# Kernel tuning notes

Hardware: AMD Instinct MI355X
Metric: run time of the kernel (lower is better)

## Reference

```python
import jax, jax.numpy as jnp
import numpy as np

B, C, H, W = 32, 48, 64, 128
K = 5  # conv kernel size (1x5 / 5x1)


def _conv1d(x, w, b):
    # x: [B, C, L]; w: [O, I, K]; b: [O]. 'same' conv (pad 2) along L.
    y = jax.lax.conv_general_dilated(x, w, window_strides=(1,), padding=[(2, 2)],
                                     dimension_numbers=("NCH", "OIH", "NCH"))
    return y + b[None, :, None]


def setup_inputs() -> dict:
    key = jax.random.key(0)
    ks = jax.random.split(key, 7)
    s = 0.02  # small init so the 64/128-step linear recurrences stay bounded
    return {
        "x": jax.random.normal(ks[0], (B, C, H, W), dtype=jnp.float32),
        "down_w": jax.random.normal(ks[1], (C, C, K), dtype=jnp.float32) * s,
        "down_b": jax.random.normal(ks[2], (C,), dtype=jnp.float32) * s,
        "right_w": jax.random.normal(ks[3], (C, C, K), dtype=jnp.float32) * s,
        "right_b": jax.random.normal(ks[4], (C,), dtype=jnp.float32) * s,
        "left_w": jax.random.normal(ks[5], (C, C, K), dtype=jnp.float32) * s,
        "left_b": jax.random.normal(ks[6], (C,), dtype=jnp.float32) * s,
    }


def reference(x, down_w, down_b, right_w, right_b, left_w, left_b):
    Bb, Cc, Hh, Ww = x.shape

    def step(w, b):
        def f(carry, inp):
            nxt = inp + _conv1d(carry, w, b)
            return nxt, nxt
        return f

    # --- down pass: d[0]=x[0]; d[t]=x[t]+down_conv(d[t-1]) ---
    xs = jnp.moveaxis(x, 2, 0)                       # [H, B, C, W]
    d0 = xs[0]
    _, d_rest = jax.lax.scan(step(down_w, down_b), d0, xs[1:])
    D = jnp.concatenate([d0[None], d_rest], 0)       # [H, B, C, W]

    # --- up pass: faithfully uses down_conv (source quirk) with index H-3-t
    # u[0]=D[H-1]; u[k]=D[H-2-k]+down_conv(u[k-1]), k=1..H-1 (H-2-k=-1 -> D[H-1])
    seq = jnp.concatenate([D[Hh - 3::-1], D[Hh - 1:Hh]], 0)  # [H-1, B, C, W]
    u0 = D[Hh - 1]
    _, u_rest = jax.lax.scan(step(down_w, down_b), u0, seq)
    U = jnp.concatenate([u0[None], u_rest], 0)[::-1]  # U[i] = u[H-1-i]

    # --- right pass over width: r[0]=U[...,0]; r[t]=U[...,t]+right_conv(r[t-1]) ---
    ws = jnp.moveaxis(jnp.moveaxis(U, 0, 2), 3, 0)   # [W, B, C, H]
    r0 = ws[0]
    _, r_rest = jax.lax.scan(step(right_w, right_b), r0, ws[1:])
    R = jnp.concatenate([r0[None], r_rest], 0)       # [W, B, C, H]

    # --- left pass (reverse): l[0]=R[W-1]; l[k]=R[W-1-k]+left_conv(l[k-1]) ---
    l0 = R[Ww - 1]
    _, l_rest = jax.lax.scan(step(left_w, left_b), l0, R[Ww - 2::-1])
    L = jnp.concatenate([l0[None], l_rest], 0)[::-1]  # [W, B, C, H]

    return jnp.moveaxis(L, 0, 3)                     # [B, C, H, W]
```

## Files before the change

kernel.cpp:

```cpp
#include <hip/hip_runtime.h>
#include <hip/hip_bf16.h>

#define B_ 32
#define C_ 48
#define H_ 64
#define W_ 128
#define K_ 5
#define SLAB (C_*H_*W_)
#define RS 56
#define ROWS 136
#define CBUF (ROWS*RS)
#define WC (W_*C_)
#define HC (H_*C_)
#define KBN 16
#define C1ROW 135

typedef __attribute__((ext_vector_type(8))) short short8;
typedef __attribute__((ext_vector_type(16))) float f32x16;
typedef unsigned short ushort;

__device__ __forceinline__ void lbar() {
  asm volatile("s_waitcnt lgkmcnt(0)\n\ts_barrier" ::: "memory");
}

__device__ __forceinline__ unsigned short f2bf(float f) {
  union { float f; unsigned u; } v; v.f = f;
  unsigned r = v.u + 0x7fffu + ((v.u >> 16) & 1u);
  return (unsigned short)(r >> 16);
}

__device__ __forceinline__ unsigned pk2(float a, float b) {
  union { __hip_bfloat162 h; unsigned u; } z;
  z.h = __float22bfloat162_rn(float2{a, b});
  return z.u;
}

template<int NMT>
__device__ __forceinline__ void load_wA32(const float* __restrict__ wgt,
                                          const float* __restrict__ bias,
                                          short8 Aw[NMT][KBN], int mt0,
                                          int l31, int h) {
#pragma unroll
  for (int mti = 0; mti < NMT; ++mti) {
    const int m = (mt0 + mti) * 32 + l31;
#pragma unroll
    for (int kbn = 0; kbn < KBN; ++kbn) {
      short8 f;
#pragma unroll
      for (int j = 0; j < 8; ++j) {
        int kp = kbn * 16 + h * 8 + j;
        float val = 0.f;
        if (m < C_) {
          if (kp < 240) {
            int k = kp / 48, i = kp - 48 * k;
            val = wgt[m * (C_ * K_) + i * K_ + k];
          } else if (kp == 240) {
            val = bias[m];
          }
        }
        f[j] = (short)f2bf(val);
      }
      Aw[mti][kbn] = f;
    }
  }
}

__device__ __forceinline__ void loadx6(float4 xv[6], const float* __restrict__ inp,
                                       size_t inRS, int n0, int l31, int h4) {
  const float* ip = inp + (size_t)(n0 + l31) * inRS + h4;
  xv[0] = *(const float4*)(ip + 0);
  xv[1] = *(const float4*)(ip + 8);
  xv[2] = *(const float4*)(ip + 16);
  xv[3] = *(const float4*)(ip + 24);
  xv[4] = *(const float4*)(ip + 32);
  xv[5] = *(const float4*)(ip + 40);
}

__device__ __forceinline__ void stepW32(const ushort* __restrict__ scr,
                                        ushort* __restrict__ scw,
                                        const short8 Aw[2][KBN],
                                        const float4 xvc[6], float4 xvn[6],
                                        const float* __restrict__ inpn, size_t inRS,
                                        float* __restrict__ outp,
                                        int n0, int l31, int h4,
                                        const int off_r[KBN], int c1off) {
  f32x16 a00 = (f32x16)(0.0f), a01 = (f32x16)(0.0f);
  f32x16 a10 = (f32x16)(0.0f), a11 = (f32x16)(0.0f);
  const ushort* bp = scr + (size_t)n0 * RS;
#pragma unroll
  for (int kbn = 0; kbn < KBN; ++kbn) {
    int off = (kbn == 15) ? c1off : off_r[kbn];
    short8 pf = *(const short8*)(bp + off);
    if (kbn & 1) {
      a01 = __builtin_amdgcn_mfma_f32_32x32x16_bf16(Aw[0][kbn], pf, a01, 0, 0, 0);
      a11 = __builtin_amdgcn_mfma_f32_32x32x16_bf16(Aw[1][kbn], pf, a11, 0, 0, 0);
    } else {
      a00 = __builtin_amdgcn_mfma_f32_32x32x16_bf16(Aw[0][kbn], pf, a00, 0, 0, 0);
      a10 = __builtin_amdgcn_mfma_f32_32x32x16_bf16(Aw[1][kbn], pf, a10, 0, 0, 0);
    }
  }
  loadx6(xvn, inpn, inRS, n0, l31, h4);
  __builtin_amdgcn_sched_barrier(0);

  const int row = n0 + l31;
  float* op = outp + (size_t)row * C_ + h4;
  ushort* wp = scw + (size_t)(row + 2) * RS + h4;
#pragma unroll
  for (int grp = 0; grp < 6; ++grp) {
    const int g = (grp < 4) ? grp : (grp - 4);
    const int ch = ((grp < 4) ? 0 : 32) + 8 * g;
    float4 v;
    if (grp < 4) {
      v.x = a00[4*g+0] + a01[4*g+0] + xvc[grp].x;
      v.y = a00[4*g+1] + a01[4*g+1] + xvc[grp].y;
      v.z = a00[4*g+2] + a01[4*g+2] + xvc[grp].z;
      v.w = a00[4*g+3] + a01[4*g+3] + xvc[grp].w;
    } else {
      v.x = a10[4*g+0] + a11[4*g+0] + xvc[grp].x;
      v.y = a10[4*g+1] + a11[4*g+1] + xvc[grp].y;
      v.z = a10[4*g+2] + a11[4*g+2] + xvc[grp].z;
      v.w = a10[4*g+3] + a11[4*g+3] + xvc[grp].w;
    }
    *(float4*)(op + ch) = v;
    uint2 pk; pk.x = pk2(v.x, v.y); pk.y = pk2(v.z, v.w);
    *(uint2*)(wp + ch) = pk;
  }
  lbar();
}

template<int MT>
__device__ __forceinline__ void stepH32(const ushort* __restrict__ scr,
                                        ushort* __restrict__ scw,
                                        const short8 Aw[KBN],
                                        const float4 xvc[4], float4 xvn[4],
                                        const float* __restrict__ inpn, size_t inRS,
                                        float* __restrict__ outp,
                                        int n0, int l31, int h4,
                                        const int off_r[KBN], int c1off) {
  constexpr int NG = MT ? 2 : 4;
  f32x16 a0 = (f32x16)(0.0f), a1 = (f32x16)(0.0f);
  f32x16 a2 = (f32x16)(0.0f), a3 = (f32x16)(0.0f);
  const ushort* bp = scr + (size_t)n0 * RS;
#pragma unroll
  for (int kbn = 0; kbn < KBN; ++kbn) {
    int off = (kbn == 15) ? c1off : off_r[kbn];
    short8 pf = *(const short8*)(bp + off);
    switch (kbn & 3) {
      case 0: a0 = __builtin_amdgcn_mfma_f32_32x32x16_bf16(Aw[kbn], pf, a0, 0, 0, 0); break;
      case 1: a1 = __builtin_amdgcn_mfma_f32_32x32x16_bf16(Aw[kbn], pf, a1, 0, 0, 0); break;
      case 2: a2 = __builtin_amdgcn_mfma_f32_32x32x16_bf16(Aw[kbn], pf, a2, 0, 0, 0); break;
      default: a3 = __builtin_amdgcn_mfma_f32_32x32x16_bf16(Aw[kbn], pf, a3, 0, 0, 0); break;
    }
  }
  const int row = n0 + l31;
  {
    const float* ip = inpn + (size_t)row * inRS + MT * 32 + h4;
#pragma unroll
    for (int g = 0; g < NG; ++g) xvn[g] = *(const float4*)(ip + 8 * g);
  }
  __builtin_amdgcn_sched_barrier(0);

  float* op = outp + (size_t)row * C_ + MT * 32 + h4;
  ushort* wp = scw + (size_t)(row + 2) * RS + MT * 32 + h4;
#pragma unroll
  for (int g = 0; g < NG; ++g) {
    float4 v;
    v.x = a0[4*g+0] + a1[4*g+0] + a2[4*g+0] + a3[4*g+0] + xvc[g].x;
    v.y = a0[4*g+1] + a1[4*g+1] + a2[4*g+1] + a3[4*g+1] + xvc[g].y;
    v.z = a0[4*g+2] + a1[4*g+2] + a2[4*g+2] + a3[4*g+2] + xvc[g].z;
    v.w = a0[4*g+3] + a1[4*g+3] + a2[4*g+3] + a3[4*g+3] + xvc[g].w;
    *(float4*)(op + 8 * g) = v;
    uint2 pk; pk.x = pk2(v.x, v.y); pk.y = pk2(v.z, v.w);
    *(uint2*)(wp + 8 * g) = pk;
  }
  lbar();
}

__device__ __forceinline__ void initW(ushort* __restrict__ scw,
                                      const float* __restrict__ inp, size_t inRS,
                                      float* __restrict__ outp,
                                      int n0, int l31, int h4) {
  const int row = n0 + l31;
  const float* ip = inp + (size_t)row * inRS + h4;
  float* op = outp + (size_t)row * C_ + h4;
  ushort* wp = scw + (size_t)(row + 2) * RS + h4;
#pragma unroll
  for (int grp = 0; grp < 6; ++grp) {
    const int g = (grp < 4) ? grp : (grp - 4);
    const int ch = ((grp < 4) ? 0 : 32) + 8 * g;
    float4 v = *(const float4*)(ip + ch);
    *(float4*)(op + ch) = v;
    uint2 pk; pk.x = pk2(v.x, v.y); pk.y = pk2(v.z, v.w);
    *(uint2*)(wp + ch) = pk;
  }
  lbar();
}

template<int MT>
__device__ __forceinline__ void initH(ushort* __restrict__ scw,
                                      const float* __restrict__ inp, size_t inRS,
                                      float* __restrict__ outp,
                                      int n0, int l31, int h4) {
  constexpr int NG = MT ? 2 : 4;
  const int row = n0 + l31;
  const float* ip = inp + (size_t)row * inRS + MT * 32 + h4;
  float* op = outp + (size_t)row * C_ + MT * 32 + h4;
  ushort* wp = scw + (size_t)(row + 2) * RS + MT * 32 + h4;
#pragma unroll
  for (int g = 0; g < NG; ++g) {
    float4 v = *(const float4*)(ip + 8 * g);
    *(float4*)(op + 8 * g) = v;
    uint2 pk; pk.x = pk2(v.x, v.y); pk.y = pk2(v.z, v.w);
    *(uint2*)(wp + 8 * g) = pk;
  }
  lbar();
}

template<class FIN, class FOUT>
__device__ __forceinline__ void run_passW(ushort* sb, int& p,
                                          const short8 Aw[2][KBN],
                                          const int off_r[KBN], int c1off,
                                          int nsteps, FIN inadr, size_t inRS, FOUT outadr,
                                          int n0, int l31, int h4) {
  float4 xa[6], xb[6];
  loadx6(xa, inadr(1), inRS, n0, l31, h4);
  for (int s = 1; s <= nsteps; s += 2) {
    {
      int sn = (s + 1 <= nsteps) ? s + 1 : nsteps;
      stepW32(sb + (size_t)p * CBUF, sb + (size_t)(p ^ 1) * CBUF, Aw, xa, xb,
              inadr(sn), inRS, outadr(s), n0, l31, h4, off_r, c1off);
      p ^= 1;
    }
    if (s + 1 <= nsteps) {
      int sn = (s + 2 <= nsteps) ? s + 2 : nsteps;
      stepW32(sb + (size_t)p * CBUF, sb + (size_t)(p ^ 1) * CBUF, Aw, xb, xa,
              inadr(sn), inRS, outadr(s + 1), n0, l31, h4, off_r, c1off);
      p ^= 1;
    }
  }
}

template<int MT, class FIN, class FOUT>
__device__ __forceinline__ void run_passH(ushort* sb, int& p,
                                          const short8 Aw[KBN],
                                          const int off_r[KBN], int c1off,
                                          int nsteps, FIN inadr, size_t inRS, FOUT outadr,
                                          int n0, int l31, int h4) {
  float4 xa[4], xb[4];
  {
    const float* ip = inadr(1) + (size_t)(n0 + l31) * inRS + MT * 32 + h4;
#pragma unroll
    for (int g = 0; g < (MT ? 2 : 4); ++g) xa[g] = *(const float4*)(ip + 8 * g);
  }
  for (int s = 1; s <= nsteps; s += 2) {
    {
      int sn = (s + 1 <= nsteps) ? s + 1 : nsteps;
      stepH32<MT>(sb + (size_t)p * CBUF, sb + (size_t)(p ^ 1) * CBUF, Aw, xa, xb,
                  inadr(sn), inRS, outadr(s), n0, l31, h4, off_r, c1off);
      p ^= 1;
    }
    if (s + 1 <= nsteps) {
      int sn = (s + 2 <= nsteps) ? s + 2 : nsteps;
      stepH32<MT>(sb + (size_t)p * CBUF, sb + (size_t)(p ^ 1) * CBUF, Aw, xb, xa,
                  inadr(sn), inRS, outadr(s + 1), n0, l31, h4, off_r, c1off);
      p ^= 1;
    }
  }
}

__device__ __forceinline__ void zero_carry_c1(ushort* sb, int tid) {
  unsigned* z = (unsigned*)sb;
  for (int i = tid; i < CBUF; i += 256) z[i] = 0u;
  __syncthreads();
  if (tid == 0) { sb[C1ROW * RS] = 0x3F80; sb[CBUF + C1ROW * RS] = 0x3F80; }
}

__global__ __launch_bounds__(256, 1) void scnn_mfma(
    float* ws,
    const float* __restrict__ dw, const float* __restrict__ db,
    const float* __restrict__ rw, const float* __restrict__ rb,
    const float* __restrict__ lw, const float* __restrict__ lb,
    float* __restrict__ DU)
{
  __shared__ __align__(32) ushort sb[2 * CBUF];
  const int tid = threadIdx.x, lane = tid & 63, wid = tid >> 6;
  const int l31 = lane & 31, h = lane >> 5, h4 = h * 4;
  const int b = blockIdx.x;
  float* xbuf = ws + (size_t)b * SLAB;
  float* rl   = ws + (size_t)b * SLAB;
  float* du   = DU + (size_t)b * SLAB;

  int off_r[KBN];
#pragma unroll
  for (int kbn = 0; kbn < 15; ++kbn) {
    int s = kbn * 16 + h * 8;
    int k = s / 48, i0 = s - 48 * k;
    off_r[kbn] = (l31 + k) * RS + i0;
  }
  off_r[15] = 0;

  const int n0w = wid * 32;
  const int ntH = wid & 1, mtH = wid >> 1;
  const int n0h = ntH * 32;
  const int c1w = (C1ROW - n0w) * RS;
  const int c1h = (C1ROW - n0h) * RS;

  int p = 0;

  {
    short8 Aw[2][KBN];
    load_wA32<2>(dw, db, Aw, 0, l31, h);
    zero_carry_c1(sb, tid);
    __syncthreads();
    initW(sb, xbuf, (size_t)C_, du, n0w, l31, h4);
    run_passW(sb, p, Aw, off_r, c1w, H_ - 1,
              [&](int s) { return xbuf + (size_t)s * WC; }, (size_t)C_,
              [&](int s) { return du + (size_t)s * WC; }, n0w, l31, h4);
    __syncthreads();
    run_passW(sb, p, Aw, off_r, c1w, H_ - 1,
              [&](int s) { int ih = (s <= H_ - 2) ? (H_ - 2 - s) : (H_ - 1);
                           return du + (size_t)ih * WC; }, (size_t)C_,
              [&](int s) { return du + (size_t)(H_ - 1 - s) * WC; }, n0w, l31, h4);
    __syncthreads();
  }

  {
    short8 Ah[1][KBN];
    load_wA32<1>(rw, rb, Ah, mtH, l31, h);
    zero_carry_c1(sb, tid);
    __syncthreads();
    p = 0;
    if (mtH == 0) initH<0>(sb, du, (size_t)WC, rl, n0h, l31, h4);
    else          initH<1>(sb, du, (size_t)WC, rl, n0h, l31, h4);
    if (mtH == 0)
      run_passH<0>(sb, p, Ah[0], off_r, c1h, W_ - 1,
                   [&](int s) { return du + (size_t)s * C_; }, (size_t)WC,
                   [&](int s) { return rl + (size_t)s * HC; }, n0h, l31, h4);
    else
      run_passH<1>(sb, p, Ah[0], off_r, c1h, W_ - 1,
                   [&](int s) { return du + (size_t)s * C_; }, (size_t)WC,
                   [&](int s) { return rl + (size_t)s * HC; }, n0h, l31, h4);
    __syncthreads();
    load_wA32<1>(lw, lb, Ah, mtH, l31, h);
    if (mtH == 0)
      run_passH<0>(sb, p, Ah[0], off_r, c1h, W_ - 1,
                   [&](int s) { return rl + (size_t)(W_ - 1 - s) * HC; }, (size_t)C_,
                   [&](int s) { return rl + (size_t)(W_ - 1 - s) * HC; }, n0h, l31, h4);
    else
      run_passH<1>(sb, p, Ah[0], off_r, c1h, W_ - 1,
                   [&](int s) { return rl + (size_t)(W_ - 1 - s) * HC; }, (size_t)C_,
                   [&](int s) { return rl + (size_t)(W_ - 1 - s) * HC; }, n0h, l31, h4);
  }
}

__global__ __launch_bounds__(256) void xpose_chw_hwc(const float* __restrict__ x,
                                                     float* __restrict__ xT) {
  __shared__ float t[C_ * 129];
  const int bh = blockIdx.x, b = bh >> 6, hh = bh & 63;
  const float* src = x + (size_t)b * SLAB + (size_t)hh * W_;
  float* dst = xT + (size_t)b * SLAB + (size_t)hh * (W_ * C_);
  for (int i = threadIdx.x; i < C_ * W_; i += 256) {
    int c = i >> 7, w = i & 127;
    t[c * 129 + w] = src[(size_t)c * (H_ * W_) + w];
  }
  __syncthreads();
  for (int i = threadIdx.x; i < C_ * W_; i += 256) {
    int w = i / C_, c = i - w * C_;
    dst[i] = t[c * 129 + w];
  }
}

__global__ __launch_bounds__(256) void xpose_whc_chw(const float* __restrict__ L,
                                                     float* __restrict__ out) {
  __shared__ float t[W_ * 49];
  const int bh = blockIdx.x, b = bh >> 6, hh = bh & 63;
  const float* src = L + (size_t)b * SLAB + (size_t)hh * C_;
  float* dst = out + (size_t)b * SLAB + (size_t)hh * W_;
  for (int i = threadIdx.x; i < W_ * C_; i += 256) {
    int w = i / C_, c = i - w * C_;
    t[w * 49 + c] = src[(size_t)w * (H_ * C_) + c];
  }
  __syncthreads();
  for (int i = threadIdx.x; i < C_ * W_; i += 256) {
    int c = i >> 7, w = i & 127;
    dst[(size_t)c * (H_ * W_) + w] = t[w * 49 + c];
  }
}

extern "C" void kernel_launch(void* const* d_in, const int* in_sizes, int n_in,
                              void* d_out, int out_size, void* d_ws, size_t ws_size,
                              hipStream_t stream) {
  const float* x  = (const float*)d_in[0];
  const float* dw = (const float*)d_in[1];
  const float* db = (const float*)d_in[2];
  const float* rw = (const float*)d_in[3];
  const float* rb = (const float*)d_in[4];
  const float* lw = (const float*)d_in[5];
  const float* lb = (const float*)d_in[6];
  float* DU = (float*)d_out;
  float* WS = (float*)d_ws;

  xpose_chw_hwc<<<B_ * H_, 256, 0, stream>>>(x, WS);
  scnn_mfma<<<B_, 256, 0, stream>>>(WS, dw, db, rw, rb, lw, lb, DU);
  xpose_whc_chw<<<B_ * H_, 256, 0, stream>>>(WS, DU);
}
```

Baseline: 436.3 us.

## Use 16x16x32 MFMA tiles for width passes with bias in accumulator init

The right and left passes over width (H=64 rows, C=48 channels) now use 16x16x32 bf16 MFMAs. Each wave owns 16 rows and all three 16-channel M tiles, replacing the 32x32 tiles that split channels 32+16 across waves and padded the M dimension. The bias is now loaded into the accumulator at init instead of going through a constant-1 carry row in the K dimension, which cuts K from 256 to 240. The next-step input loads are issued before the MFMA chain, and a sched_barrier keeps them there. This removes padded wasted MFMA work in the H passes, at the cost of more weight registers (24 short8 per lane) and a different numeric accumulation order.

```diff
diff --git a/kernel.cpp b/kernel.cpp
--- a/kernel.cpp
+++ b/kernel.cpp
@@ -12,10 +12,12 @@
 #define CBUF (ROWS*RS)
 #define WC (W_*C_)
 #define HC (H_*C_)
-#define KBN 16
+#define KB32 16
+#define KB16 8
 #define C1ROW 135
 
 typedef __attribute__((ext_vector_type(8))) short short8;
+typedef __attribute__((ext_vector_type(4))) float f32x4;
 typedef __attribute__((ext_vector_type(16))) float f32x16;
 typedef unsigned short ushort;
 
@@ -35,20 +37,18 @@
   return z.u;
 }
 
-template<int NMT>
 __device__ __forceinline__ void load_wA32(const float* __restrict__ wgt,
                                           const float* __restrict__ bias,
-                                          short8 Aw[NMT][KBN], int mt0,
-                                          int l31, int h) {
-#pragma unroll
-  for (int mti = 0; mti < NMT; ++mti) {
-    const int m = (mt0 + mti) * 32 + l31;
-#pragma unroll
-    for (int kbn = 0; kbn < KBN; ++kbn) {
+                                          short8 Aw[2][KB32], int l31, int hh) {
+#pragma unroll
+  for (int mti = 0; mti < 2; ++mti) {
+    const int m = mti * 32 + l31;
+#pragma unroll
+    for (int kbn = 0; kbn < KB32; ++kbn) {
       short8 f;
 #pragma unroll
       for (int j = 0; j < 8; ++j) {
-        int kp = kbn * 16 + h * 8 + j;
+        int kp = kbn * 16 + hh * 8 + j;
         float val = 0.f;
         if (m < C_) {
           if (kp < 240) {
@@ -78,18 +78,18 @@
 
 __device__ __forceinline__ void stepW32(const ushort* __restrict__ scr,
                                         ushort* __restrict__ scw,
-                                        const short8 Aw[2][KBN],
+                                        const short8 Aw[2][KB32],
                                         const float4 xvc[6], float4 xvn[6],
                                         const float* __restrict__ inpn, size_t inRS,
                                         float* __restrict__ outp,
                                         int n0, int l31, int h4,
-                                        const int off_r[KBN], int c1off) {
+                                        const int off32[KB32], int c1off) {
   f32x16 a00 = (f32x16)(0.0f), a01 = (f32x16)(0.0f);
   f32x16 a10 = (f32x16)(0.0f), a11 = (f32x16)(0.0f);
   const ushort* bp = scr + (size_t)n0 * RS;
 #pragma unroll
-  for (int kbn = 0; kbn < KBN; ++kbn) {
-    int off = (kbn == 15) ? c1off : off_r[kbn];
+  for (int kbn = 0; kbn < KB32; ++kbn) {
+    int off = (kbn == 15) ? c1off : off32[kbn];
     short8 pf = *(const short8*)(bp + off);
     if (kbn & 1) {
       a01 = __builtin_amdgcn_mfma_f32_32x32x16_bf16(Aw[0][kbn], pf, a01, 0, 0, 0);
@@ -128,54 +128,6 @@
   lbar();
 }
 
-template<int MT>
-__device__ __forceinline__ void stepH32(const ushort* __restrict__ scr,
-                                        ushort* __restrict__ scw,
-                                        const short8 Aw[KBN],
-                                        const float4 xvc[4], float4 xvn[4],
-                                        const float* __restrict__ inpn, size_t inRS,
-                                        float* __restrict__ outp,
-                                        int n0, int l31, int h4,
-                                        const int off_r[KBN], int c1off) {
-  constexpr int NG = MT ? 2 : 4;
-  f32x16 a0 = (f32x16)(0.0f), a1 = (f32x16)(0.0f);
-  f32x16 a2 = (f32x16)(0.0f), a3 = (f32x16)(0.0f);
-  const ushort* bp = scr + (size_t)n0 * RS;
-#pragma unroll
-  for (int kbn = 0; kbn < KBN; ++kbn) {
-    int off = (kbn == 15) ? c1off : off_r[kbn];
-    short8 pf = *(const short8*)(bp + off);
-    switch (kbn & 3) {
-      case 0: a0 = __builtin_amdgcn_mfma_f32_32x32x16_bf16(Aw[kbn], pf, a0, 0, 0, 0); break;
-      case 1: a1 = __builtin_amdgcn_mfma_f32_32x32x16_bf16(Aw[kbn], pf, a1, 0, 0, 0); break;
-      case 2: a2 = __builtin_amdgcn_mfma_f32_32x32x16_bf16(Aw[kbn], pf, a2, 0, 0, 0); break;
-      default: a3 = __builtin_amdgcn_mfma_f32_32x32x16_bf16(Aw[kbn], pf, a3, 0, 0, 0); break;
-    }
-  }
-  const int row = n0 + l31;
-  {
-    const float* ip = inpn + (size_t)row * inRS + MT * 32 + h4;
-#pragma unroll
-    for (int g = 0; g < NG; ++g) xvn[g] = *(const float4*)(ip + 8 * g);
-  }
-  __builtin_amdgcn_sched_barrier(0);
-
-  float* op = outp + (size_t)row * C_ + MT * 32 + h4;
-  ushort* wp = scw + (size_t)(row + 2) * RS + MT * 32 + h4;
-#pragma unroll
-  for (int g = 0; g < NG; ++g) {
-    float4 v;
-    v.x = a0[4*g+0] + a1[4*g+0] + a2[4*g+0] + a3[4*g+0] + xvc[g].x;
-    v.y = a0[4*g+1] + a1[4*g+1] + a2[4*g+1] + a3[4*g+1] + xvc[g].y;
-    v.z = a0[4*g+2] + a1[4*g+2] + a2[4*g+2] + a3[4*g+2] + xvc[g].z;
-    v.w = a0[4*g+3] + a1[4*g+3] + a2[4*g+3] + a3[4*g+3] + xvc[g].w;
-    *(float4*)(op + 8 * g) = v;
-    uint2 pk; pk.x = pk2(v.x, v.y); pk.y = pk2(v.z, v.w);
-    *(uint2*)(wp + 8 * g) = pk;
-  }
-  lbar();
-}
-
 __device__ __forceinline__ void initW(ushort* __restrict__ scw,
                                       const float* __restrict__ inp, size_t inRS,
                                       float* __restrict__ outp,
@@ -196,30 +148,10 @@
   lbar();
 }
 
-template<int MT>
-__device__ __forceinline__ void initH(ushort* __restrict__ scw,
-                                      const float* __restrict__ inp, size_t inRS,
-                                      float* __restrict__ outp,
-                                      int n0, int l31, int h4) {
-  constexpr int NG = MT ? 2 : 4;
-  const int row = n0 + l31;
-  const float* ip = inp + (size_t)row * inRS + MT * 32 + h4;
-  float* op = outp + (size_t)row * C_ + MT * 32 + h4;
-  ushort* wp = scw + (size_t)(row + 2) * RS + MT * 32 + h4;
-#pragma unroll
-  for (int g = 0; g < NG; ++g) {
-    float4 v = *(const float4*)(ip + 8 * g);
-    *(float4*)(op + 8 * g) = v;
-    uint2 pk; pk.x = pk2(v.x, v.y); pk.y = pk2(v.z, v.w);
-    *(uint2*)(wp + 8 * g) = pk;
-  }
-  lbar();
-}
-
 template<class FIN, class FOUT>
 __device__ __forceinline__ void run_passW(ushort* sb, int& p,
-                                          const short8 Aw[2][KBN],
-                                          const int off_r[KBN], int c1off,
+                                          const short8 Aw[2][KB32],
+                                          const int off32[KB32], int c1off,
                                           int nsteps, FIN inadr, size_t inRS, FOUT outadr,
                                           int n0, int l31, int h4) {
   float4 xa[6], xb[6];
@@ -228,51 +160,128 @@
     {
       int sn = (s + 1 <= nsteps) ? s + 1 : nsteps;
       stepW32(sb + (size_t)p * CBUF, sb + (size_t)(p ^ 1) * CBUF, Aw, xa, xb,
-              inadr(sn), inRS, outadr(s), n0, l31, h4, off_r, c1off);
+              inadr(sn), inRS, outadr(s), n0, l31, h4, off32, c1off);
       p ^= 1;
     }
     if (s + 1 <= nsteps) {
       int sn = (s + 2 <= nsteps) ? s + 2 : nsteps;
       stepW32(sb + (size_t)p * CBUF, sb + (size_t)(p ^ 1) * CBUF, Aw, xb, xa,
-              inadr(sn), inRS, outadr(s + 1), n0, l31, h4, off_r, c1off);
+              inadr(sn), inRS, outadr(s + 1), n0, l31, h4, off32, c1off);
       p ^= 1;
     }
   }
 }
 
-template<int MT, class FIN, class FOUT>
+__device__ __forceinline__ void load_wA16(const float* __restrict__ wgt,
+                                          const float* __restrict__ bias,
+                                          short8 Ah[3][KB16], f32x4 bv[3],
+                                          int l15, int q8, int c0) {
+#pragma unroll
+  for (int mt = 0; mt < 3; ++mt) {
+#pragma unroll
+    for (int r = 0; r < 4; ++r) bv[mt][r] = bias[mt * 16 + c0 + r];
+#pragma unroll
+    for (int kb = 0; kb < KB16; ++kb) {
+      short8 f;
+#pragma unroll
+      for (int j = 0; j < 8; ++j) {
+        int kp = kb * 32 + q8 + j;
+        int k = kp / 48, i = kp - 48 * k;
+        f[j] = (kp < 240)
+             ? (short)f2bf(wgt[(mt * 16 + l15) * (C_ * K_) + i * K_ + k])
+             : (short)0;
+      }
+      Ah[mt][kb] = f;
+    }
+  }
+}
+
+__device__ __forceinline__ void load_xin1(float4 xv[3], const float* __restrict__ inp,
+                                          size_t lRS, int n0, int l15, int c0) {
+  const float* p = inp + (size_t)(n0 + l15) * lRS + c0;
+#pragma unroll
+  for (int mt = 0; mt < 3; ++mt) xv[mt] = *(const float4*)(p + mt * 16);
+}
+
+__device__ __forceinline__ void stepH16(const ushort* __restrict__ scr,
+                                        ushort* __restrict__ scw,
+                                        const short8 Ah[3][KB16], const f32x4 bv[3],
+                                        const float4 xv[3], const int off16[KB16],
+                                        float* __restrict__ outp,
+                                        int n0, int l15, int c0) {
+  f32x4 acc[4][3];
+#pragma unroll
+  for (int s = 0; s < 4; ++s)
+#pragma unroll
+    for (int mt = 0; mt < 3; ++mt)
+      acc[s][mt] = (s == 0) ? bv[mt] : (f32x4){0.f, 0.f, 0.f, 0.f};
+
+#pragma unroll
+  for (int kb = 0; kb < KB16; ++kb) {
+    short8 pf = *(const short8*)(scr + (size_t)n0 * RS + off16[kb]);
+#pragma unroll
+    for (int mt = 0; mt < 3; ++mt)
+      acc[kb % 4][mt] = __builtin_amdgcn_mfma_f32_16x16x32_bf16(
+          Ah[mt][kb], pf, acc[kb % 4][mt], 0, 0, 0);
+  }
+
+  const int row = n0 + l15;
+#pragma unroll
+  for (int mt = 0; mt < 3; ++mt) {
+    float4 v;
+    v.x = acc[0][mt][0] + acc[1][mt][0] + acc[2][mt][0] + acc[3][mt][0] + xv[mt].x;
+    v.y = acc[0][mt][1] + acc[1][mt][1] + acc[2][mt][1] + acc[3][mt][1] + xv[mt].y;
+    v.z = acc[0][mt][2] + acc[1][mt][2] + acc[2][mt][2] + acc[3][mt][2] + xv[mt].z;
+    v.w = acc[0][mt][3] + acc[1][mt][3] + acc[2][mt][3] + acc[3][mt][3] + xv[mt].w;
+    *(float4*)(outp + (size_t)row * C_ + mt * 16 + c0) = v;
+    uint2 pk; pk.x = pk2(v.x, v.y); pk.y = pk2(v.z, v.w);
+    *(uint2*)(scw + (size_t)(row + 2) * RS + mt * 16 + c0) = pk;
+  }
+  lbar();
+}
+
+__device__ __forceinline__ void initH16(ushort* __restrict__ scw,
+                                        const float* __restrict__ inp, size_t lRS,
+                                        float* __restrict__ outp,
+                                        int n0, int l15, int c0) {
+  const int row = n0 + l15;
+  const float* p = inp + (size_t)row * lRS + c0;
+#pragma unroll
+  for (int mt = 0; mt < 3; ++mt) {
+    float4 v = *(const float4*)(p + mt * 16);
+    *(float4*)(outp + (size_t)row * C_ + mt * 16 + c0) = v;
+    uint2 pk; pk.x = pk2(v.x, v.y); pk.y = pk2(v.z, v.w);
+    *(uint2*)(scw + (size_t)(row + 2) * RS + mt * 16 + c0) = pk;
+  }
+  lbar();
+}
+
+template<class FIN, class FOUT>
 __device__ __forceinline__ void run_passH(ushort* sb, int& p,
-                                          const short8 Aw[KBN],
-                                          const int off_r[KBN], int c1off,
-                                          int nsteps, FIN inadr, size_t inRS, FOUT outadr,
-                                          int n0, int l31, int h4) {
-  float4 xa[4], xb[4];
-  {
-    const float* ip = inadr(1) + (size_t)(n0 + l31) * inRS + MT * 32 + h4;
-#pragma unroll
-    for (int g = 0; g < (MT ? 2 : 4); ++g) xa[g] = *(const float4*)(ip + 8 * g);
-  }
+                                          const short8 Ah[3][KB16], const f32x4 bv[3],
+                                          const int off16[KB16],
+                                          int nsteps, FIN inadr, size_t lRS, FOUT outadr,
+                                          int n0, int l15, int c0) {
+  float4 xa[3], xb[3];
+  load_xin1(xa, inadr(1), lRS, n0, l15, c0);
   for (int s = 1; s <= nsteps; s += 2) {
     {
       int sn = (s + 1 <= nsteps) ? s + 1 : nsteps;
-      stepH32<MT>(sb + (size_t)p * CBUF, sb + (size_t)(p ^ 1) * CBUF, Aw, xa, xb,
-                  inadr(sn), inRS, outadr(s), n0, l31, h4, off_r, c1off);
+      load_xin1(xb, inadr(sn), lRS, n0, l15, c0);
+      __builtin_amdgcn_sched_barrier(0x38F);
+      stepH16(sb + (size_t)p * CBUF, sb + (size_t)(p ^ 1) * CBUF,
+              Ah, bv, xa, off16, outadr(s), n0, l15, c0);
       p ^= 1;
     }
     if (s + 1 <= nsteps) {
       int sn = (s + 2 <= nsteps) ? s + 2 : nsteps;
-      stepH32<MT>(sb + (size_t)p * CBUF, sb + (size_t)(p ^ 1) * CBUF, Aw, xb, xa,
-                  inadr(sn), inRS, outadr(s + 1), n0, l31, h4, off_r, c1off);
+      load_xin1(xa, inadr(sn), lRS, n0, l15, c0);
+      __builtin_amdgcn_sched_barrier(0x38F);
+      stepH16(sb + (size_t)p * CBUF, sb + (size_t)(p ^ 1) * CBUF,
+              Ah, bv, xb, off16, outadr(s + 1), n0, l15, c0);
       p ^= 1;
     }
   }
-}
-
-__device__ __forceinline__ void zero_carry_c1(ushort* sb, int tid) {
-  unsigned* z = (unsigned*)sb;
-  for (int i = tid; i < CBUF; i += 256) z[i] = 0u;
-  __syncthreads();
-  if (tid == 0) { sb[C1ROW * RS] = 0x3F80; sb[CBUF + C1ROW * RS] = 0x3F80; }
 }
 
 __global__ __launch_bounds__(256, 1) void scnn_mfma(
@@ -284,40 +293,46 @@
 {
   __shared__ __align__(32) ushort sb[2 * CBUF];
   const int tid = threadIdx.x, lane = tid & 63, wid = tid >> 6;
-  const int l31 = lane & 31, h = lane >> 5, h4 = h * 4;
+  const int l31 = lane & 31, hh = lane >> 5, h4 = hh * 4;
+  const int l15 = lane & 15, q = lane >> 4, q8 = q * 8, c0 = 4 * q;
   const int b = blockIdx.x;
   float* xbuf = ws + (size_t)b * SLAB;
   float* rl   = ws + (size_t)b * SLAB;
   float* du   = DU + (size_t)b * SLAB;
 
-  int off_r[KBN];
+  int off32[KB32];
 #pragma unroll
   for (int kbn = 0; kbn < 15; ++kbn) {
-    int s = kbn * 16 + h * 8;
+    int s = kbn * 16 + hh * 8;
     int k = s / 48, i0 = s - 48 * k;
-    off_r[kbn] = (l31 + k) * RS + i0;
-  }
-  off_r[15] = 0;
-
-  const int n0w = wid * 32;
-  const int ntH = wid & 1, mtH = wid >> 1;
-  const int n0h = ntH * 32;
+    off32[kbn] = (l31 + k) * RS + i0;
+  }
+  off32[15] = 0;
+  int off16[KB16];
+#pragma unroll
+  for (int kb = 0; kb < KB16; ++kb) {
+    int s = kb * 32 + q8;
+    int k = s / 48, i0 = s - 48 * k;
+    off16[kb] = (l15 + k) * RS + i0;
+  }
+
+  const int n0w = wid * 32, n0h = wid * 16;
   const int c1w = (C1ROW - n0w) * RS;
-  const int c1h = (C1ROW - n0h) * RS;
-
   int p = 0;
 
   {
-    short8 Aw[2][KBN];
-    load_wA32<2>(dw, db, Aw, 0, l31, h);
-    zero_carry_c1(sb, tid);
+    short8 Aw[2][KB32];
+    load_wA32(dw, db, Aw, l31, hh);
+    { unsigned* z = (unsigned*)sb; for (int i = tid; i < CBUF; i += 256) z[i] = 0u; }
+    __syncthreads();
+    if (tid == 0) { sb[C1ROW * RS] = 0x3F80; sb[CBUF + C1ROW * RS] = 0x3F80; }
     __syncthreads();
     initW(sb, xbuf, (size_t)C_, du, n0w, l31, h4);
-    run_passW(sb, p, Aw, off_r, c1w, H_ - 1,
+    run_passW(sb, p, Aw, off32, c1w, H_ - 1,
               [&](int s) { return xbuf + (size_t)s * WC; }, (size_t)C_,
               [&](int s) { return du + (size_t)s * WC; }, n0w, l31, h4);
     __syncthreads();
-    run_passW(sb, p, Aw, off_r, c1w, H_ - 1,
+    run_passW(sb, p, Aw, off32, c1w, H_ - 1,
               [&](int s) { int ih = (s <= H_ - 2) ? (H_ - 2 - s) : (H_ - 1);
                            return du + (size_t)ih * WC; }, (size_t)C_,
               [&](int s) { return du + (size_t)(H_ - 1 - s) * WC; }, n0w, l31, h4);
@@ -325,40 +340,30 @@
   }
 
   {
-    short8 Ah[1][KBN];
-    load_wA32<1>(rw, rb, Ah, mtH, l31, h);
-    zero_carry_c1(sb, tid);
+    short8 Ah[3][KB16];
+    f32x4 bv[3];
+    load_wA16(rw, rb, Ah, bv, l15, q8, c0);
+    { unsigned* z = (unsigned*)sb; for (int i = tid; i < CBUF; i += 256) z[i] = 0u; }
     __syncthreads();
     p = 0;
-    if (mtH == 0) initH<0>(sb, du, (size_t)WC, rl, n0h, l31, h4);
-    else          initH<1>(sb, du, (size_t)WC, rl, n0h, l31, h4);
-    if (mtH == 0)
-      run_passH<0>(sb, p, Ah[0], off_r, c1h, W_ - 1,
-                   [&](int s) { return du + (size_t)s * C_; }, (size_t)WC,
-                   [&](int s) { return rl + (size_t)s * HC; }, n0h, l31, h4);
-    else
-      run_passH<1>(sb, p, Ah[0], off_r, c1h, W_ - 1,
-                   [&](int s) { return du + (size_t)s * C_; }, (size_t)WC,
-                   [&](int s) { return rl + (size_t)s * HC; }, n0h, l31, h4);
-    __syncthreads();
-    load_wA32<1>(lw, lb, Ah, mtH, l31, h);
-    if (mtH == 0)
-      run_passH<0>(sb, p, Ah[0], off_r, c1h, W_ - 1,
-                   [&](int s) { return rl + (size_t)(W_ - 1 - s) * HC; }, (size_t)C_,
-                   [&](int s) { return rl + (size_t)(W_ - 1 - s) * HC; }, n0h, l31, h4);
-    else
-      run_passH<1>(sb, p, Ah[0], off_r, c1h, W_ - 1,
-                   [&](int s) { return rl + (size_t)(W_ - 1 - s) * HC; }, (size_t)C_,
-                   [&](int s) { return rl + (size_t)(W_ - 1 - s) * HC; }, n0h, l31, h4);
+    initH16(sb, du, (size_t)WC, rl, n0h, l15, c0);
+    run_passH(sb, p, Ah, bv, off16, W_ - 1,
+              [&](int s) { return du + (size_t)s * C_; }, (size_t)WC,
+              [&](int s) { return rl + (size_t)s * HC; }, n0h, l15, c0);
+    __syncthreads();
+    load_wA16(lw, lb, Ah, bv, l15, q8, c0);
+    run_passH(sb, p, Ah, bv, off16, W_ - 1,
+              [&](int s) { return rl + (size_t)(W_ - 1 - s) * HC; }, (size_t)C_,
+              [&](int s) { return rl + (size_t)(W_ - 1 - s) * HC; }, n0h, l15, c0);
   }
 }
 
 __global__ __launch_bounds__(256) void xpose_chw_hwc(const float* __restrict__ x,
                                                      float* __restrict__ xT) {
   __shared__ float t[C_ * 129];
-  const int bh = blockIdx.x, b = bh >> 6, hh = bh & 63;
-  const float* src = x + (size_t)b * SLAB + (size_t)hh * W_;
-  float* dst = xT + (size_t)b * SLAB + (size_t)hh * (W_ * C_);
+  const int bh = blockIdx.x, b = bh >> 6, hrow = bh & 63;
+  const float* src = x + (size_t)b * SLAB + (size_t)hrow * W_;
+  float* dst = xT + (size_t)b * SLAB + (size_t)hrow * (W_ * C_);
   for (int i = threadIdx.x; i < C_ * W_; i += 256) {
     int c = i >> 7, w = i & 127;
     t[c * 129 + w] = src[(size_t)c * (H_ * W_) + w];
@@ -373,9 +378,9 @@
 __global__ __launch_bounds__(256) void xpose_whc_chw(const float* __restrict__ L,
                                                      float* __restrict__ out) {
   __shared__ float t[W_ * 49];
-  const int bh = blockIdx.x, b = bh >> 6, hh = bh & 63;
-  const float* src = L + (size_t)b * SLAB + (size_t)hh * C_;
-  float* dst = out + (size_t)b * SLAB + (size_t)hh * W_;
+  const int bh = blockIdx.x, b = bh >> 6, hrow = bh & 63;
+  const float* src = L + (size_t)b * SLAB + (size_t)hrow * C_;
+  float* dst = out + (size_t)b * SLAB + (size_t)hrow * W_;
   for (int i = threadIdx.x; i < W_ * C_; i += 256) {
     int w = i / C_, c = i - w * C_;
     t[w * 49 + c] = src[(size_t)w * (H_ * C_) + c];
```

New measurement: 429.0 us. No clear change (-1.7%).
